# Performance work log

Measured on AMD Instinct MI355X. Metric: run time of the kernel, lower is better.

## Reference

```python
import jax, jax.numpy as jnp
import numpy as np

N = 8192      # num nodes
E = 262144    # num edges (avg degree 32)
IN = 512
HID = 512
LAT = 128


def setup_inputs() -> dict:
    key = jax.random.key(0)
    ks = jax.random.split(key, 8)
    edge_index = jax.random.randint(ks[0], (2, E), 0, N, dtype=jnp.int64 if jax.config.read('jax_enable_x64') else jnp.int32)
    x = jax.random.normal(ks[1], (N, IN), jnp.float32)
    def w(k, i, o):
        return jax.random.normal(k, (i, o), jnp.float32) * (1.0 / np.sqrt(i))
    return {
        'edge_index': edge_index,
        'x': x,
        'W1': w(ks[2], IN, HID), 'b1': jnp.zeros((HID,), jnp.float32),
        'Wmu': w(ks[3], HID, LAT), 'bmu': jnp.zeros((LAT,), jnp.float32),
        'Wlv': w(ks[4], HID, LAT), 'blv': jnp.zeros((LAT,), jnp.float32),
    }


def gcn_conv(x, row, col, W, b):
    # PyG GCNConv: h = x W; symmetric norm with self-loops (added by caller);
    # out[i] = sum_{(j->i)} d_j^{-1/2} d_i^{-1/2} h[j] + b
    h = x @ W
    ones = jnp.ones((row.shape[0],), h.dtype)
    deg = jax.ops.segment_sum(ones, col, num_segments=N)  # in-degree incl. self-loop
    dinv_sqrt = jnp.where(deg > 0, jax.lax.rsqrt(jnp.maximum(deg, 1e-12)), 0.0)
    norm = dinv_sqrt[row] * dinv_sqrt[col]                # [E+N]
    out = jax.ops.segment_sum(norm[:, None] * h[row], col, num_segments=N)
    return out + b


def reference(edge_index, x, W1, b1, Wmu, bmu, Wlv, blv):
    # add self-loops once, reuse for all layers
    loops = jnp.arange(N, dtype=edge_index.dtype)
    row = jnp.concatenate([edge_index[0], loops])
    col = jnp.concatenate([edge_index[1], loops])

    h = jax.nn.relu(gcn_conv(x, row, col, W1, b1))
    mu = gcn_conv(h, row, col, Wmu, bmu)
    logvar = gcn_conv(h, row, col, Wlv, blv)
    z = mu  # eval-mode reparameterize (deterministic)
    A_pred = jax.nn.sigmoid(z @ z.T)  # [N, N] dot-product decode
    return (A_pred, mu, logvar, z)
```

## Files before the change

kernel.cpp:

```cpp
#include <hip/hip_runtime.h>

#define NNODES 8192
#define NEDGES 262144
#define FIN 512
#define FHID 512
#define FLAT 128

typedef unsigned short bfu;
typedef __attribute__((ext_vector_type(8))) short short8;
typedef __attribute__((ext_vector_type(4))) float f32x4;
typedef __attribute__((ext_vector_type(4))) unsigned short us4;

__device__ __forceinline__ float bf2f(unsigned short u) {
    union { unsigned int i; float f; } c; c.i = ((unsigned int)u) << 16; return c.f;
}
__device__ __forceinline__ unsigned short f2bf(float f) {
    union { float f; unsigned int i; } c; c.f = f;
    unsigned int i = c.i;
    unsigned int r = (i + 0x7FFFu + ((i >> 16) & 1u)) >> 16;
    return (unsigned short)r;
}

__global__ void k_zero(int* p, int n) {
    int i = blockIdx.x * blockDim.x + threadIdx.x;
    if (i < n) p[i] = 0;
}

__global__ void k_count(const int* __restrict__ ei, int* __restrict__ deg) {
    int e = blockIdx.x * blockDim.x + threadIdx.x;
    if (e < NEDGES) atomicAdd(&deg[ei[NEDGES + e]], 1);
}

__global__ void k_scan(const int* __restrict__ deg, int* __restrict__ row_start,
                       float* __restrict__ dinv) {
    __shared__ int part[256];
    int t = threadIdx.x, base = t * 32;
    int s = 0;
    for (int i = 0; i < 32; i++) s += deg[base + i];
    part[t] = s;
    __syncthreads();
    for (int off = 1; off < 256; off <<= 1) {
        int v = (t >= off) ? part[t - off] : 0;
        __syncthreads();
        part[t] += v;
        __syncthreads();
    }
    int run = (t == 0) ? 0 : part[t - 1];
    for (int i = 0; i < 32; i++) {
        int d = deg[base + i];
        row_start[base + i] = run;
        run += d;
        dinv[base + i] = rsqrtf((float)(d + 1));
    }
    if (t == 255) row_start[NNODES] = run;
}

__global__ void k_scatter(const int* __restrict__ ei, const int* __restrict__ row_start,
                          int* __restrict__ cursor, int* __restrict__ csr) {
    int e = blockIdx.x * blockDim.x + threadIdx.x;
    if (e < NEDGES) {
        int dst = ei[NEDGES + e];
        int p = atomicAdd(&cursor[dst], 1);
        csr[row_start[dst] + p] = ei[e];
    }
}

__global__ void k_wcsr(const int* __restrict__ csr, const float* __restrict__ dinv,
                       float* __restrict__ wcsr) {
    int p = blockIdx.x * blockDim.x + threadIdx.x;
    if (p < NEDGES) wcsr[p] = dinv[csr[p]];
}

__global__ void k_cvt_x(const float* __restrict__ x, bfu* __restrict__ xb) {
    int i = blockIdx.x * blockDim.x + threadIdx.x;
    const float4 v = ((const float4*)x)[i];
    ushort2 lo = {f2bf(v.x), f2bf(v.y)};
    ushort2 hi = {f2bf(v.z), f2bf(v.w)};
    ((ushort2*)xb)[2 * i] = lo;
    ((ushort2*)xb)[2 * i + 1] = hi;
}

__global__ void k_bt(const float* __restrict__ W1, const float* __restrict__ Wmu,
                     const float* __restrict__ Wlv, bfu* __restrict__ Bt1, bfu* __restrict__ Bt2) {
    int idx = blockIdx.x * blockDim.x + threadIdx.x;
    if (idx < 512 * 512) {
        int n = idx >> 9, k = idx & 511;
        Bt1[idx] = f2bf(W1[k * 512 + n]);
    } else if (idx < 512 * 512 + 256 * 512) {
        int j = idx - 512 * 512;
        int n = j >> 9, k = j & 511;
        Bt2[j] = f2bf((n < 128) ? Wmu[k * 128 + n] : Wlv[k * 128 + (n - 128)]);
    }
}

template <int ACT, int TM, int TN, typename CT>
__global__ void k_gemm_nt(const bfu* __restrict__ A, const bfu* __restrict__ Bt,
                          CT* __restrict__ C, int M, int N, int K) {
    int wid  = (blockIdx.x * blockDim.x + threadIdx.x) >> 6;
    int lane = threadIdx.x & 63;
    int l = lane & 15, q = lane >> 4;
    int tn = N / (16 * TN);
    int m0 = (wid / tn) * (16 * TM), n0 = (wid % tn) * (16 * TN);

    f32x4 acc[TM][TN];
#pragma unroll
    for (int a = 0; a < TM; a++)
#pragma unroll
        for (int b = 0; b < TN; b++) acc[a][b] = (f32x4){0.f, 0.f, 0.f, 0.f};

    const bfu* Ap = A + (size_t)(m0 + l) * K + q * 8;
    const bfu* Bp = Bt + (size_t)(n0 + l) * K + q * 8;

    for (int k0 = 0; k0 < K; k0 += 32) {
        short8 av[TM], bv[TN];
#pragma unroll
        for (int mi = 0; mi < TM; mi++)
            av[mi] = *(const short8*)(Ap + (size_t)mi * 16 * K + k0);
#pragma unroll
        for (int ni = 0; ni < TN; ni++)
            bv[ni] = *(const short8*)(Bp + (size_t)ni * 16 * K + k0);
#pragma unroll
        for (int mi = 0; mi < TM; mi++)
#pragma unroll
            for (int ni = 0; ni < TN; ni++)
                acc[mi][ni] = __builtin_amdgcn_mfma_f32_16x16x32_bf16(bv[ni], av[mi],
                                                                     acc[mi][ni], 0, 0, 0);
    }

#pragma unroll
    for (int mi = 0; mi < TM; mi++) {
        int row = m0 + mi * 16 + l;
#pragma unroll
        for (int ni = 0; ni < TN; ni++) {
            int col = n0 + ni * 16 + q * 4;
            f32x4 v = acc[mi][ni];
            if (ACT == 2) {
#pragma unroll
                for (int r = 0; r < 4; r++)
                    v[r] = __builtin_amdgcn_rcpf(1.0f + __expf(-v[r]));
            }
            if constexpr (sizeof(CT) == 2) {
                us4 o = {f2bf(v[0]), f2bf(v[1]), f2bf(v[2]), f2bf(v[3])};
                *(us4*)(C + (size_t)row * N + col) = o;
            } else {
                *(f32x4*)(C + (size_t)row * N + col) = v;
            }
        }
    }
}

template <int F>
__device__ __forceinline__ void agg_core(const bfu* __restrict__ hin,
                                         const int* __restrict__ csr,
                                         const float* __restrict__ wcsr,
                                         int s, int e, int i, int f, float di,
                                         float& a0, float& a1) {
    a0 = 0.f; a1 = 0.f;
    int ed = s;
    for (; ed + 4 <= e; ed += 4) {
        int s0 = csr[ed], s1 = csr[ed + 1], s2 = csr[ed + 2], s3 = csr[ed + 3];
        float w0 = wcsr[ed], w1 = wcsr[ed + 1], w2 = wcsr[ed + 2], w3 = wcsr[ed + 3];
        unsigned int p0 = *(const unsigned int*)(hin + (size_t)s0 * F + f);
        unsigned int p1 = *(const unsigned int*)(hin + (size_t)s1 * F + f);
        unsigned int p2 = *(const unsigned int*)(hin + (size_t)s2 * F + f);
        unsigned int p3 = *(const unsigned int*)(hin + (size_t)s3 * F + f);
        a0 += w0 * bf2f((unsigned short)(p0 & 0xFFFF));
        a1 += w0 * bf2f((unsigned short)(p0 >> 16));
        a0 += w1 * bf2f((unsigned short)(p1 & 0xFFFF));
        a1 += w1 * bf2f((unsigned short)(p1 >> 16));
        a0 += w2 * bf2f((unsigned short)(p2 & 0xFFFF));
        a1 += w2 * bf2f((unsigned short)(p2 >> 16));
        a0 += w3 * bf2f((unsigned short)(p3 & 0xFFFF));
        a1 += w3 * bf2f((unsigned short)(p3 >> 16));
    }
    for (; ed < e; ed++) {
        int src = csr[ed];
        float w = wcsr[ed];
        unsigned int pk = *(const unsigned int*)(hin + (size_t)src * F + f);
        a0 += w * bf2f((unsigned short)(pk & 0xFFFF));
        a1 += w * bf2f((unsigned short)(pk >> 16));
    }
    unsigned int pk = *(const unsigned int*)(hin + (size_t)i * F + f);
    a0 += di * bf2f((unsigned short)(pk & 0xFFFF));
    a1 += di * bf2f((unsigned short)(pk >> 16));
}

__global__ void k_agg1(const bfu* __restrict__ hin, const int* __restrict__ csr,
                       const float* __restrict__ wcsr, const int* __restrict__ rs,
                       const float* __restrict__ dinv, const float* __restrict__ bias,
                       bfu* __restrict__ hout) {
    int i = blockIdx.x;
    int f = threadIdx.x * 2;
    float di = dinv[i];
    float a0, a1;
    agg_core<FHID>(hin, csr, wcsr, rs[i], rs[i + 1], i, f, di, a0, a1);
    float o0 = fmaxf(di * a0 + bias[f], 0.f);
    float o1 = fmaxf(di * a1 + bias[f + 1], 0.f);
    unsigned int outw = (unsigned int)f2bf(o0) | ((unsigned int)f2bf(o1) << 16);
    *(unsigned int*)(hout + (size_t)i * FHID + f) = outw;
}

__global__ void k_agg2(const bfu* __restrict__ hin, const int* __restrict__ csr,
                       const float* __restrict__ wcsr, const int* __restrict__ rs,
                       const float* __restrict__ dinv, const float* __restrict__ bmu,
                       const float* __restrict__ blv, float* __restrict__ out_mu,
                       float* __restrict__ out_lv, float* __restrict__ out_z,
                       bfu* __restrict__ ws_z) {
    int i = blockIdx.x;
    int f = threadIdx.x * 2;
    float di = dinv[i];
    float a0, a1;
    agg_core<256>(hin, csr, wcsr, rs[i], rs[i + 1], i, f, di, a0, a1);
    float v0 = di * a0, v1 = di * a1;
    if (f < 128) {
        v0 += bmu[f]; v1 += bmu[f + 1];
        float2 fv = {v0, v1};
        *(float2*)(out_mu + (size_t)i * FLAT + f) = fv;
        *(float2*)(out_z + (size_t)i * FLAT + f) = fv;
        unsigned int bw = (unsigned int)f2bf(v0) | ((unsigned int)f2bf(v1) << 16);
        *(unsigned int*)(ws_z + (size_t)i * FLAT + f) = bw;
    } else {
        int fl = f - 128;
        v0 += blv[fl]; v1 += blv[fl + 1];
        float2 fv = {v0, v1};
        *(float2*)(out_lv + (size_t)i * FLAT + fl) = fv;
    }
}

extern "C" void kernel_launch(void* const* d_in, const int* in_sizes, int n_in,
                              void* d_out, int out_size, void* d_ws, size_t ws_size,
                              hipStream_t stream) {
    const int*   ei  = (const int*)d_in[0];
    const float* x   = (const float*)d_in[1];
    const float* W1  = (const float*)d_in[2];
    const float* b1  = (const float*)d_in[3];
    const float* Wmu = (const float*)d_in[4];
    const float* bmu = (const float*)d_in[5];
    const float* Wlv = (const float*)d_in[6];
    const float* blv = (const float*)d_in[7];
    float* out = (float*)d_out;

    char* wsb = (char*)d_ws;
    size_t off = 0;
    auto alloc = [&](size_t bytes) -> char* {
        char* p = wsb + off;
        off += (bytes + 255) & ~(size_t)255;
        return p;
    };
    int*   deg       = (int*)alloc(NNODES * 4);
    int*   cursor    = (int*)alloc(NNODES * 4);
    int*   row_start = (int*)alloc((NNODES + 1) * 4);
    float* dinv      = (float*)alloc(NNODES * 4);
    int*   csr       = (int*)alloc(NEDGES * 4);
    float* wcsr      = (float*)alloc(NEDGES * 4);
    bfu*   Bt1       = (bfu*)alloc(512 * 512 * 2);
    bfu*   Bt2       = (bfu*)alloc(256 * 512 * 2);
    bfu*   xb        = (bfu*)alloc((size_t)NNODES * FIN * 2);
    bfu*   h0        = (bfu*)alloc((size_t)NNODES * FHID * 2);
    bfu*   h         = (bfu*)alloc((size_t)NNODES * FHID * 2);
    bfu*   hml       = (bfu*)alloc((size_t)NNODES * 256 * 2);
    bfu*   zb        = (bfu*)alloc((size_t)NNODES * FLAT * 2);

    float* out_mu = out + (size_t)NNODES * NNODES;
    float* out_lv = out_mu + (size_t)NNODES * FLAT;
    float* out_z  = out_lv + (size_t)NNODES * FLAT;

    k_zero<<<(2 * NNODES + 255) / 256, 256, 0, stream>>>(deg, 2 * NNODES);
    k_count<<<NEDGES / 256, 256, 0, stream>>>(ei, deg);
    k_scan<<<1, 256, 0, stream>>>(deg, row_start, dinv);
    k_scatter<<<NEDGES / 256, 256, 0, stream>>>(ei, row_start, cursor, csr);
    k_wcsr<<<NEDGES / 256, 256, 0, stream>>>(csr, dinv, wcsr);
    k_bt<<<(512 * 512 + 256 * 512) / 256, 256, 0, stream>>>(W1, Wmu, Wlv, Bt1, Bt2);
    k_cvt_x<<<(NNODES * FIN / 4) / 256, 256, 0, stream>>>(x, xb);

    k_gemm_nt<0, 4, 2, bfu><<<(8192 / 64) * (512 / 32) / 4, 256, 0, stream>>>(
        xb, Bt1, h0, 8192, 512, 512);
    k_agg1<<<NNODES, 256, 0, stream>>>(h0, csr, wcsr, row_start, dinv, b1, h);

    k_gemm_nt<0, 2, 2, bfu><<<(8192 / 32) * (256 / 32) / 4, 256, 0, stream>>>(
        h, Bt2, hml, 8192, 256, 512);
    k_agg2<<<NNODES, 128, 0, stream>>>(hml, csr, wcsr, row_start, dinv, bmu, blv,
                                       out_mu, out_lv, out_z, zb);

    k_gemm_nt<2, 4, 4, float><<<(8192 / 64) * (8192 / 64) / 4, 256, 0, stream>>>(
        zb, zb, out, 8192, 8192, 128);
}
```

Measured before the change: 478.0 us.

## Fuse wcsr into scatter, tile weight transposes, use nontemporal output stores

Folds the edge-weight gather into the CSR scatter kernel, which removes one launch and a re-read of csr. Replaces the strided weight-transpose kernel with LDS-tiled 32x32 transposes so both global reads and writes are coalesced. Switches the large fp32 output stores (the 8192x8192 sigmoid matrix and the mu/logvar/z outputs) to nontemporal stores to reduce cache pollution. These are small setup-path and store-path tweaks; the dominant cost is writing the 256MB A_pred matrix.

```diff
diff --git a/kernel.cpp b/kernel.cpp
--- a/kernel.cpp
+++ b/kernel.cpp
@@ -9,6 +9,7 @@
 typedef unsigned short bfu;
 typedef __attribute__((ext_vector_type(8))) short short8;
 typedef __attribute__((ext_vector_type(4))) float f32x4;
+typedef __attribute__((ext_vector_type(2))) float f32x2;
 typedef __attribute__((ext_vector_type(4))) unsigned short us4;
 
 __device__ __forceinline__ float bf2f(unsigned short u) {
@@ -56,19 +57,17 @@
 }
 
 __global__ void k_scatter(const int* __restrict__ ei, const int* __restrict__ row_start,
-                          int* __restrict__ cursor, int* __restrict__ csr) {
+                          int* __restrict__ cursor, int* __restrict__ csr,
+                          const float* __restrict__ dinv, float* __restrict__ wcsr) {
     int e = blockIdx.x * blockDim.x + threadIdx.x;
     if (e < NEDGES) {
+        int src = ei[e];
         int dst = ei[NEDGES + e];
         int p = atomicAdd(&cursor[dst], 1);
-        csr[row_start[dst] + p] = ei[e];
-    }
-}
-
-__global__ void k_wcsr(const int* __restrict__ csr, const float* __restrict__ dinv,
-                       float* __restrict__ wcsr) {
-    int p = blockIdx.x * blockDim.x + threadIdx.x;
-    if (p < NEDGES) wcsr[p] = dinv[csr[p]];
+        int pos = row_start[dst] + p;
+        csr[pos] = src;
+        wcsr[pos] = dinv[src];
+    }
 }
 
 __global__ void k_cvt_x(const float* __restrict__ x, bfu* __restrict__ xb) {
@@ -80,17 +79,35 @@
     ((ushort2*)xb)[2 * i + 1] = hi;
 }
 
-__global__ void k_bt(const float* __restrict__ W1, const float* __restrict__ Wmu,
-                     const float* __restrict__ Wlv, bfu* __restrict__ Bt1, bfu* __restrict__ Bt2) {
-    int idx = blockIdx.x * blockDim.x + threadIdx.x;
-    if (idx < 512 * 512) {
-        int n = idx >> 9, k = idx & 511;
-        Bt1[idx] = f2bf(W1[k * 512 + n]);
-    } else if (idx < 512 * 512 + 256 * 512) {
-        int j = idx - 512 * 512;
-        int n = j >> 9, k = j & 511;
-        Bt2[j] = f2bf((n < 128) ? Wmu[k * 128 + n] : Wlv[k * 128 + (n - 128)]);
-    }
+__global__ void k_bt1_t(const float* __restrict__ W, bfu* __restrict__ Bt) {
+    __shared__ bfu tile[32][33];
+    int tx = threadIdx.x & 31, ty = threadIdx.x >> 5;
+    int nb = blockIdx.x & 15, kb = blockIdx.x >> 4;
+    int n0 = nb * 32, k0 = kb * 32;
+#pragma unroll
+    for (int i = 0; i < 32; i += 8)
+        tile[ty + i][tx] = f2bf(W[(size_t)(k0 + ty + i) * 512 + n0 + tx]);
+    __syncthreads();
+#pragma unroll
+    for (int i = 0; i < 32; i += 8)
+        Bt[(size_t)(n0 + ty + i) * 512 + k0 + tx] = tile[tx][ty + i];
+}
+
+__global__ void k_bt2_t(const float* __restrict__ Wmu, const float* __restrict__ Wlv,
+                        bfu* __restrict__ Bt) {
+    __shared__ bfu tile[32][33];
+    int tx = threadIdx.x & 31, ty = threadIdx.x >> 5;
+    int nb = blockIdx.x & 7, kb = blockIdx.x >> 3;
+    int n0 = nb * 32, k0 = kb * 32;
+    const float* Wsel = (n0 < 128) ? Wmu : Wlv;
+    int noff = (n0 < 128) ? 0 : 128;
+#pragma unroll
+    for (int i = 0; i < 32; i += 8)
+        tile[ty + i][tx] = f2bf(Wsel[(size_t)(k0 + ty + i) * 128 + (n0 + tx - noff)]);
+    __syncthreads();
+#pragma unroll
+    for (int i = 0; i < 32; i += 8)
+        Bt[(size_t)(n0 + ty + i) * 512 + k0 + tx] = tile[tx][ty + i];
 }
 
 template <int ACT, int TM, int TN, typename CT>
@@ -143,7 +160,7 @@
                 us4 o = {f2bf(v[0]), f2bf(v[1]), f2bf(v[2]), f2bf(v[3])};
                 *(us4*)(C + (size_t)row * N + col) = o;
             } else {
-                *(f32x4*)(C + (size_t)row * N + col) = v;
+                __builtin_nontemporal_store(v, (f32x4*)(C + (size_t)row * N + col));
             }
         }
     }
@@ -214,16 +231,16 @@
     float v0 = di * a0, v1 = di * a1;
     if (f < 128) {
         v0 += bmu[f]; v1 += bmu[f + 1];
-        float2 fv = {v0, v1};
-        *(float2*)(out_mu + (size_t)i * FLAT + f) = fv;
-        *(float2*)(out_z + (size_t)i * FLAT + f) = fv;
+        f32x2 fv = {v0, v1};
+        __builtin_nontemporal_store(fv, (f32x2*)(out_mu + (size_t)i * FLAT + f));
+        __builtin_nontemporal_store(fv, (f32x2*)(out_z + (size_t)i * FLAT + f));
         unsigned int bw = (unsigned int)f2bf(v0) | ((unsigned int)f2bf(v1) << 16);
         *(unsigned int*)(ws_z + (size_t)i * FLAT + f) = bw;
     } else {
         int fl = f - 128;
         v0 += blv[fl]; v1 += blv[fl + 1];
-        float2 fv = {v0, v1};
-        *(float2*)(out_lv + (size_t)i * FLAT + fl) = fv;
+        f32x2 fv = {v0, v1};
+        __builtin_nontemporal_store(fv, (f32x2*)(out_lv + (size_t)i * FLAT + fl));
     }
 }
 
@@ -268,9 +285,9 @@
     k_zero<<<(2 * NNODES + 255) / 256, 256, 0, stream>>>(deg, 2 * NNODES);
     k_count<<<NEDGES / 256, 256, 0, stream>>>(ei, deg);
     k_scan<<<1, 256, 0, stream>>>(deg, row_start, dinv);
-    k_scatter<<<NEDGES / 256, 256, 0, stream>>>(ei, row_start, cursor, csr);
-    k_wcsr<<<NEDGES / 256, 256, 0, stream>>>(csr, dinv, wcsr);
-    k_bt<<<(512 * 512 + 256 * 512) / 256, 256, 0, stream>>>(W1, Wmu, Wlv, Bt1, Bt2);
+    k_scatter<<<NEDGES / 256, 256, 0, stream>>>(ei, row_start, cursor, csr, dinv, wcsr);
+    k_bt1_t<<<256, 256, 0, stream>>>(W1, Bt1);
+    k_bt2_t<<<128, 256, 0, stream>>>(Wmu, Wlv, Bt2);
     k_cvt_x<<<(NNODES * FIN / 4) / 256, 256, 0, stream>>>(x, xb);
 
     k_gemm_nt<0, 4, 2, bfu><<<(8192 / 64) * (512 / 32) / 4, 256, 0, stream>>>(
```

Result: no change. 486.5 us (+1.8%).
